# Performance work log

Measured on AMD Instinct MI355X. Metric: run time of the kernel, lower is better.

The kernel has to match this reference:

```python
import jax, jax.numpy as jnp
import numpy as np

IN_FEATURES = 4096
OUT_FEATURES = 4096
NNZ = 1677721  # int(4096*4096*(1-0.9))


def setup_inputs() -> dict:
    key = jax.random.key(0)
    k1, k2, k3, k4 = jax.random.split(key, 4)
    x = jax.random.normal(k1, (4, 2048, IN_FEATURES), dtype=jnp.float32)
    bound = 1.0 / np.sqrt(IN_FEATURES)
    sparse_values = jax.random.uniform(k2, (NNZ,), minval=-bound, maxval=bound, dtype=jnp.float32)
    bias = jax.random.uniform(k3, (OUT_FEATURES,), minval=-bound, maxval=bound, dtype=jnp.float32)
    flat_idx = jnp.sort(jax.random.randint(k4, (NNZ,), 0, IN_FEATURES * OUT_FEATURES, dtype=jnp.int64))
    return {"x": x, "sparse_values": sparse_values, "bias": bias, "flat_idx": flat_idx}


def reference(x, sparse_values, bias, flat_idx):
    # Fixed COO pattern: row = flat // in_features, col = flat % in_features
    rows = flat_idx // IN_FEATURES
    cols = flat_idx % IN_FEATURES
    # Scatter-add == COO coalesce (duplicates summed). W: [out, in]
    W = jnp.zeros((OUT_FEATURES, IN_FEATURES), dtype=sparse_values.dtype).at[rows, cols].add(sparse_values)
    # y = x W^T + b  (matches torch.sparse.mm(W, x^T)^T + b)
    y = jnp.einsum('bsi,oi->bso', x, W) + bias
    return y.astype(x.dtype)
```

## Files before the change

### kernel.cpp

```cpp
#include <hip/hip_runtime.h>
#include <hip/hip_bf16.h>
#include <stdint.h>

#define IN_F 4096
#define OUT_F 4096

typedef __attribute__((ext_vector_type(8))) __bf16 bf16x8;
typedef __attribute__((ext_vector_type(4))) float f32x4;

__device__ __forceinline__ void gl_lds_16(const void* g, void* l) {
    __builtin_amdgcn_global_load_lds((const __attribute__((address_space(1))) void*)g,
                                     (__attribute__((address_space(3))) void*)l,
                                     16, 0, 0);
}

__global__ void cvt_and_scatter(const float* __restrict__ x, __bf16* __restrict__ Xb, int n8,
                                const float* __restrict__ vals, const int* __restrict__ idx,
                                __bf16* __restrict__ W, int nnz, int cvtBlocks) {
    if ((int)blockIdx.x < cvtBlocks) {
        int i = blockIdx.x * blockDim.x + threadIdx.x;
        if (i < n8) {
            const float4* src = (const float4*)(x + (size_t)i * 8);
            float4 v0 = src[0], v1 = src[1];
            bf16x8 o;
            o[0] = (__bf16)v0.x; o[1] = (__bf16)v0.y; o[2] = (__bf16)v0.z; o[3] = (__bf16)v0.w;
            o[4] = (__bf16)v1.x; o[5] = (__bf16)v1.y; o[6] = (__bf16)v1.z; o[7] = (__bf16)v1.w;
            *(bf16x8*)(Xb + (size_t)i * 8) = o;
        }
    } else {
        int i = (blockIdx.x - cvtBlocks) * blockDim.x + threadIdx.x;
        if (i >= nnz) return;
        const int id = idx[i];
        if (i > 0 && idx[i - 1] == id) return;
        float s = vals[i];
        for (int j = i + 1; j < nnz && idx[j] == id; ++j) s += vals[j];
        W[id] = (__bf16)s;
    }
}

#define BM 256
#define BN 256
#define BK 32
#define NT (IN_F / BK)

__global__ __launch_bounds__(512, 2) void gemm_bf16_bt(
    const __bf16* __restrict__ A, const __bf16* __restrict__ B,
    const float* __restrict__ bias, float* __restrict__ C,
    int M, int N, int K)
{
    __shared__ __align__(128) __bf16 lds[4][16384];

    const int t512 = threadIdx.x;
    const int wave = t512 >> 6;
    const int lane = t512 & 63;
    const int wm = wave >> 2;
    const int wn = wave & 3;
    const int lq = lane >> 4;
    const int lr = lane & 15;

    const int bid  = blockIdx.x;
    const int wgid = (bid & 7) * 64 + (bid >> 3);
    const int mt = wgid >> 4;
    const int nt = wgid & 15;
    const int tileM = mt * BM;
    const int tileN = nt * BN;

    const int srow = t512 >> 2;
    const int scol = (t512 & 3) * 8;

    const __bf16* gA0 = A + (size_t)(tileM + srow) * K + scol;
    const __bf16* gA1 = A + (size_t)(tileM + 128 + srow) * K + scol;
    const __bf16* gB0 = B + (size_t)(tileN + srow) * K + scol;
    const __bf16* gB1 = B + (size_t)(tileN + 128 + srow) * K + scol;

#define STAGE_A(buf, k0) do { \
        gl_lds_16(gA0 + (k0), &lds[buf][0]    + t512 * 8); \
        gl_lds_16(gA1 + (k0), &lds[buf][4096] + t512 * 8); } while (0)
#define STAGE_B(buf, k0) do { \
        gl_lds_16(gB0 + (k0), &lds[buf][8192]         + t512 * 8); \
        gl_lds_16(gB1 + (k0), &lds[buf][8192 + 4096]  + t512 * 8); } while (0)

    const int aoff = (wm * 128 + lr) * BK + lq * 8;
    const int boff = 8192 + (wn * 64 + lr) * BK + lq * 8;

    f32x4 acc[8][4] = {};

    STAGE_A(0, 0);   STAGE_B(0, 0);
    STAGE_A(1, 32);  STAGE_B(1, 32);
    STAGE_A(2, 64);  STAGE_B(2, 64);
    asm volatile("s_waitcnt vmcnt(8)" ::: "memory");
    __builtin_amdgcn_s_barrier();
    asm volatile("" ::: "memory");

    for (int t = 0; t < NT; ++t) {
        const __bf16* sbuf = &lds[t & 3][0];
        const int  pk = (t + 3) * BK;
        const int  pb = (t + 3) & 3;
        const bool pf = (t + 3) < NT;

        if (pf) { STAGE_A(pb, pk); STAGE_B(pb, pk); }

        bf16x8 af[8], bg[4];
#pragma unroll
        for (int mi = 0; mi < 8; ++mi) af[mi] = *(const bf16x8*)&sbuf[aoff + mi * 512];
#pragma unroll
        for (int ni = 0; ni < 4; ++ni) bg[ni] = *(const bf16x8*)&sbuf[boff + ni * 512];

        __builtin_amdgcn_s_setprio(1);
#pragma unroll
        for (int mi = 0; mi < 8; ++mi)
#pragma unroll
            for (int ni = 0; ni < 4; ++ni)
                acc[mi][ni] = __builtin_amdgcn_mfma_f32_16x16x32_bf16(af[mi], bg[ni], acc[mi][ni], 0, 0, 0);
        __builtin_amdgcn_s_setprio(0);

        asm volatile("s_waitcnt lgkmcnt(0)" ::: "memory");
        if (t < NT - 3)       asm volatile("s_waitcnt vmcnt(8)" ::: "memory");
        else if (t == NT - 3) asm volatile("s_waitcnt vmcnt(4)" ::: "memory");
        else if (t == NT - 2) asm volatile("s_waitcnt vmcnt(0)" ::: "memory");
        __builtin_amdgcn_s_barrier();
        asm volatile("" ::: "memory");
    }

    float bv[4];
#pragma unroll
    for (int ni = 0; ni < 4; ++ni) bv[ni] = bias[tileN + wn * 64 + ni * 16 + lr];
#pragma unroll
    for (int mi = 0; mi < 8; ++mi) {
#pragma unroll
        for (int ni = 0; ni < 4; ++ni) {
            const int gn = tileN + wn * 64 + ni * 16 + lr;
#pragma unroll
            for (int r = 0; r < 4; ++r) {
                const int gm = tileM + wm * 128 + mi * 16 + lq * 4 + r;
                C[(size_t)gm * N + gn] = acc[mi][ni][r] + bv[ni];
            }
        }
    }
#undef STAGE_A
#undef STAGE_B
}

extern "C" void kernel_launch(void* const* d_in, const int* in_sizes, int n_in,
                              void* d_out, int out_size, void* d_ws, size_t ws_size,
                              hipStream_t stream) {
    const float* x    = (const float*)d_in[0];
    const float* vals = (const float*)d_in[1];
    const float* bias = (const float*)d_in[2];
    const int*   idx  = (const int*)d_in[3];
    float* out = (float*)d_out;

    const int nnz = in_sizes[1];
    const int K = IN_F, N = OUT_F;
    const int M = in_sizes[0] / K;

    char* ws = (char*)d_ws;
    __bf16* Wb = (__bf16*)ws;
    __bf16* Xb = (__bf16*)(ws + (size_t)32 * 1024 * 1024);

    const int wElems = N * K;
    const int xElems = M * K;
    const int n8 = xElems / 8;
    const int cvtBlocks = n8 / 256;
    const int scatBlocks = (nnz + 255) / 256;

    hipMemsetAsync(Wb, 0, (size_t)wElems * sizeof(__bf16), stream);
    cvt_and_scatter<<<cvtBlocks + scatBlocks, 256, 0, stream>>>(
        x, Xb, n8, vals, idx, Wb, nnz, cvtBlocks);

    gemm_bf16_bt<<<(M / BM) * (N / BN), 512, 0, stream>>>(Xb, Wb, bias, out, M, N, K);
}
```

Measured before the change: 486.8 us.

## Build dense W per segment via binary search and swizzle GEMM LDS layout

Replaces the memset plus per-nonzero scatter with a dense builder. Each block owns 2048 weight entries, binary-searches the sorted index array for its range, and each thread writes 8 bf16 values with one vector store. This drops the separate memset launch and the scattered 2-byte writes. The GEMM also XOR-swizzles the 16-byte column chunk on both the global-to-LDS staging and the fragment reads, aiming to cut LDS bank conflicts. The cost is extra binary-search loads per thread and a more complex index mapping.

```diff
diff --git a/kernel.cpp b/kernel.cpp
--- a/kernel.cpp
+++ b/kernel.cpp
@@ -14,9 +14,9 @@
                                      16, 0, 0);
 }
 
-__global__ void cvt_and_scatter(const float* __restrict__ x, __bf16* __restrict__ Xb, int n8,
-                                const float* __restrict__ vals, const int* __restrict__ idx,
-                                __bf16* __restrict__ W, int nnz, int cvtBlocks) {
+__global__ void cvt_and_build(const float* __restrict__ x, __bf16* __restrict__ Xb, int n8,
+                              const float* __restrict__ vals, const int* __restrict__ idx,
+                              __bf16* __restrict__ W, int nnz, int cvtBlocks) {
     if ((int)blockIdx.x < cvtBlocks) {
         int i = blockIdx.x * blockDim.x + threadIdx.x;
         if (i < n8) {
@@ -28,13 +28,33 @@
             *(bf16x8*)(Xb + (size_t)i * 8) = o;
         }
     } else {
-        int i = (blockIdx.x - cvtBlocks) * blockDim.x + threadIdx.x;
-        if (i >= nnz) return;
-        const int id = idx[i];
-        if (i > 0 && idx[i - 1] == id) return;
-        float s = vals[i];
-        for (int j = i + 1; j < nnz && idx[j] == id; ++j) s += vals[j];
-        W[id] = (__bf16)s;
+        const int b = (int)blockIdx.x - cvtBlocks;
+        const int s = b << 11;
+        __shared__ int slo, shi;
+        if (threadIdx.x == 0) {
+            int lo = 0, hi = nnz;
+            while (lo < hi) { int m = (lo + hi) >> 1; if (idx[m] < s) lo = m + 1; else hi = m; }
+            slo = lo;
+        }
+        if (threadIdx.x == 1) {
+            int lo = 0, hi = nnz;
+            const int e = s + 2048;
+            while (lo < hi) { int m = (lo + hi) >> 1; if (idx[m] < e) lo = m + 1; else hi = m; }
+            shi = lo;
+        }
+        __syncthreads();
+        const int ts = s + (int)threadIdx.x * 8;
+        int l = slo, h = shi;
+        while (l < h) { int m = (l + h) >> 1; if (idx[m] < ts) l = m + 1; else h = m; }
+        int j = l;
+        bf16x8 o;
+#pragma unroll
+        for (int k = 0; k < 8; ++k) {
+            float a = 0.0f;
+            while (j < shi && idx[j] == ts + k) { a += vals[j]; ++j; }
+            o[k] = (__bf16)a;
+        }
+        *(bf16x8*)(W + ts) = o;
     }
 }
 
@@ -66,7 +86,7 @@
     const int tileN = nt * BN;
 
     const int srow = t512 >> 2;
-    const int scol = (t512 & 3) * 8;
+    const int scol = ((t512 & 3) ^ ((t512 >> 3) & 3)) * 8;
 
     const __bf16* gA0 = A + (size_t)(tileM + srow) * K + scol;
     const __bf16* gA1 = A + (size_t)(tileM + 128 + srow) * K + scol;
@@ -80,8 +100,9 @@
         gl_lds_16(gB0 + (k0), &lds[buf][8192]         + t512 * 8); \
         gl_lds_16(gB1 + (k0), &lds[buf][8192 + 4096]  + t512 * 8); } while (0)
 
-    const int aoff = (wm * 128 + lr) * BK + lq * 8;
-    const int boff = 8192 + (wn * 64 + lr) * BK + lq * 8;
+    const int cswz = (lq ^ ((lr >> 1) & 3)) * 8;
+    const int aoff = (wm * 128 + lr) * BK + cswz;
+    const int boff = 8192 + (wn * 64 + lr) * BK + cswz;
 
     f32x4 acc[8][4] = {};
 
@@ -162,10 +183,9 @@
     const int xElems = M * K;
     const int n8 = xElems / 8;
     const int cvtBlocks = n8 / 256;
-    const int scatBlocks = (nnz + 255) / 256;
+    const int buildBlocks = wElems / 2048;
 
-    hipMemsetAsync(Wb, 0, (size_t)wElems * sizeof(__bf16), stream);
-    cvt_and_scatter<<<cvtBlocks + scatBlocks, 256, 0, stream>>>(
+    cvt_and_build<<<cvtBlocks + buildBlocks, 256, 0, stream>>>(
         x, Xb, n8, vals, idx, Wb, nnz, cvtBlocks);
 
     gemm_bf16_bt<<<(M / BM) * (N / BN), 512, 0, stream>>>(Xb, Wb, bias, out, M, N, K);
```

New measurement: 513.6 us. 5.5% more time.

## Swizzle LDS layout and double-buffer register fragments across K tiles

Applied to the files above, without the earlier changes.

Applies an XOR swizzle to the column chunk used when staging A/B tiles into LDS and when reading fragments, to reduce LDS bank conflicts. The main loop now loads the next tile's fragments into a second register set while MFMAs run on the current set, with sched_barrier and adjusted vmcnt waits, and unrolls by two. This hides LDS read latency behind matrix math. The cost is more VGPRs, which at 2 waves/SIMD may cause spills, and the new wait counts must still be correct.

```diff
diff --git a/kernel.cpp b/kernel.cpp
--- a/kernel.cpp
+++ b/kernel.cpp
@@ -66,7 +66,7 @@
     const int tileN = nt * BN;
 
     const int srow = t512 >> 2;
-    const int scol = (t512 & 3) * 8;
+    const int scol = ((t512 & 3) ^ ((t512 >> 3) & 3)) * 8;
 
     const __bf16* gA0 = A + (size_t)(tileM + srow) * K + scol;
     const __bf16* gA1 = A + (size_t)(tileM + 128 + srow) * K + scol;
@@ -80,46 +80,58 @@
         gl_lds_16(gB0 + (k0), &lds[buf][8192]         + t512 * 8); \
         gl_lds_16(gB1 + (k0), &lds[buf][8192 + 4096]  + t512 * 8); } while (0)
 
-    const int aoff = (wm * 128 + lr) * BK + lq * 8;
-    const int boff = 8192 + (wn * 64 + lr) * BK + lq * 8;
+    const int cswz = (lq ^ ((lr >> 1) & 3)) * 8;
+    const int aoff = (wm * 128 + lr) * BK + cswz;
+    const int boff = 8192 + (wn * 64 + lr) * BK + cswz;
 
     f32x4 acc[8][4] = {};
+    bf16x8 fa0[8], fb0[4], fa1[8], fb1[4];
+
+#define TILE(T, FAc, FBc, FAn, FBn) do {                                        \
+        const int t_ = (T);                                                     \
+        if (t_ + 3 < NT) {                                                      \
+            const int pb_ = (t_ + 3) & 3; const int pk_ = (t_ + 3) * BK;        \
+            STAGE_A(pb_, pk_); STAGE_B(pb_, pk_);                               \
+        }                                                                       \
+        if (t_ + 1 < NT) {                                                      \
+            const __bf16* nb_ = &lds[(t_ + 1) & 3][0];                          \
+            _Pragma("unroll") for (int mi = 0; mi < 8; ++mi)                    \
+                FAn[mi] = *(const bf16x8*)&nb_[aoff + mi * 512];                \
+            _Pragma("unroll") for (int ni = 0; ni < 4; ++ni)                    \
+                FBn[ni] = *(const bf16x8*)&nb_[boff + ni * 512];                \
+        }                                                                       \
+        __builtin_amdgcn_sched_barrier(0);                                      \
+        __builtin_amdgcn_s_setprio(1);                                          \
+        _Pragma("unroll") for (int mi = 0; mi < 8; ++mi)                        \
+            _Pragma("unroll") for (int ni = 0; ni < 4; ++ni)                    \
+                acc[mi][ni] = __builtin_amdgcn_mfma_f32_16x16x32_bf16(          \
+                    FAc[mi], FBc[ni], acc[mi][ni], 0, 0, 0);                    \
+        __builtin_amdgcn_s_setprio(0);                                          \
+        if (t_ < NT - 3)       asm volatile("s_waitcnt vmcnt(4)" ::: "memory"); \
+        else if (t_ == NT - 3) asm volatile("s_waitcnt vmcnt(0)" ::: "memory"); \
+        if (t_ < NT - 1) {                                                      \
+            __builtin_amdgcn_s_barrier();                                       \
+            asm volatile("" ::: "memory");                                      \
+        }                                                                       \
+    } while (0)
 
     STAGE_A(0, 0);   STAGE_B(0, 0);
     STAGE_A(1, 32);  STAGE_B(1, 32);
     STAGE_A(2, 64);  STAGE_B(2, 64);
-    asm volatile("s_waitcnt vmcnt(8)" ::: "memory");
+    asm volatile("s_waitcnt vmcnt(4)" ::: "memory");
     __builtin_amdgcn_s_barrier();
     asm volatile("" ::: "memory");
+    {
+        const __bf16* nb_ = &lds[0][0];
+#pragma unroll
+        for (int mi = 0; mi < 8; ++mi) fa0[mi] = *(const bf16x8*)&nb_[aoff + mi * 512];
+#pragma unroll
+        for (int ni = 0; ni < 4; ++ni) fb0[ni] = *(const bf16x8*)&nb_[boff + ni * 512];
+    }
 
-    for (int t = 0; t < NT; ++t) {
-        const __bf16* sbuf = &lds[t & 3][0];
-        const int  pk = (t + 3) * BK;
-        const int  pb = (t + 3) & 3;
-        const bool pf = (t + 3) < NT;
-
-        if (pf) { STAGE_A(pb, pk); STAGE_B(pb, pk); }
-
-        bf16x8 af[8], bg[4];
-#pragma unroll
-        for (int mi = 0; mi < 8; ++mi) af[mi] = *(const bf16x8*)&sbuf[aoff + mi * 512];
-#pragma unroll
-        for (int ni = 0; ni < 4; ++ni) bg[ni] = *(const bf16x8*)&sbuf[boff + ni * 512];
-
-        __builtin_amdgcn_s_setprio(1);
-#pragma unroll
-        for (int mi = 0; mi < 8; ++mi)
-#pragma unroll
-            for (int ni = 0; ni < 4; ++ni)
-                acc[mi][ni] = __builtin_amdgcn_mfma_f32_16x16x32_bf16(af[mi], bg[ni], acc[mi][ni], 0, 0, 0);
-        __builtin_amdgcn_s_setprio(0);
-
-        asm volatile("s_waitcnt lgkmcnt(0)" ::: "memory");
-        if (t < NT - 3)       asm volatile("s_waitcnt vmcnt(8)" ::: "memory");
-        else if (t == NT - 3) asm volatile("s_waitcnt vmcnt(4)" ::: "memory");
-        else if (t == NT - 2) asm volatile("s_waitcnt vmcnt(0)" ::: "memory");
-        __builtin_amdgcn_s_barrier();
-        asm volatile("" ::: "memory");
+    for (int t = 0; t < NT; t += 2) {
+        TILE(t,     fa0, fb0, fa1, fb1);
+        TILE(t + 1, fa1, fb1, fa0, fb0);
     }
 
     float bv[4];
@@ -137,6 +149,7 @@
             }
         }
     }
+#undef TILE
 #undef STAGE_A
 #undef STAGE_B
 }
```

Measured after the change: 467.2 us. 1.04x faster.
